# Kernel tuning notes

Measured on AMD Instinct MI355X. Metric: run time of the kernel, lower is better.

The kernel has to match this reference:

```python
import jax, jax.numpy as jnp
import numpy as np

EPS = 0.001

def batchnorm(x, gamma, beta):
    # x: [N, C, H, W]; training-mode batch statistics over (N, H, W), biased variance (torch BN)
    mean = jnp.mean(x, axis=(0, 2, 3), keepdims=True)
    var = jnp.mean(jnp.square(x - mean), axis=(0, 2, 3), keepdims=True)
    xn = (x - mean) * jax.lax.rsqrt(var + EPS)
    return xn * gamma[None, :, None, None] + beta[None, :, None, None]

def setup_inputs() -> dict:
    key = jax.random.key(0)
    ks = jax.random.split(key, 6)
    N, C, C2, H, W = 8, 256, 256, 96, 96
    num_heads, key_dim, value_dim = 8, 32, 32
    q_input = jax.random.normal(ks[0], (N, C, H, W), dtype=jnp.float32)
    kv = jax.random.normal(ks[1], (N, C2, H, W), dtype=jnp.float32)
    # 1x1 conv weights as matrices [out, in], kaiming-normal-ish scale
    Wq = jax.random.normal(ks[2], (key_dim * num_heads, C), dtype=jnp.float32) * np.sqrt(2.0 / C)
    Wk = jax.random.normal(ks[3], (key_dim * num_heads, C2), dtype=jnp.float32) * np.sqrt(2.0 / C2)
    Wv = jax.random.normal(ks[4], (value_dim * num_heads, C2), dtype=jnp.float32) * np.sqrt(2.0 / C2)
    Wp = jax.random.normal(ks[5], (C, value_dim * num_heads), dtype=jnp.float32) * np.sqrt(2.0 / (value_dim * num_heads))
    return {
        "q_input": q_input, "kv": kv,
        "Wq": Wq, "Wk": Wk, "Wv": Wv, "Wp": Wp,
        "q_gamma": jnp.ones((C,), jnp.float32), "q_beta": jnp.zeros((C,), jnp.float32),
        "kv_gamma": jnp.ones((C2,), jnp.float32), "kv_beta": jnp.zeros((C2,), jnp.float32),
    }

def reference(q_input, kv, Wq, Wk, Wv, Wp, q_gamma, q_beta, kv_gamma, kv_beta):
    NUM_HEADS, KEY_DIM, VALUE_DIM = 8, 32, 32
    n, C, q_h, q_w = q_input.shape
    _, C2, kv_h, kv_w = kv.shape
    Lq, Lk = q_h * q_w, kv_h * kv_w
    qn = batchnorm(q_input, q_gamma, q_beta)
    kvn = batchnorm(kv, kv_gamma, kv_beta)
    # 1x1 convs == channel matmuls; reshape to [n, heads, dim, L]
    queries = jnp.einsum('oc,nchw->nohw', Wq, qn).reshape(n, NUM_HEADS, KEY_DIM, Lq)
    keys = jnp.einsum('oc,nchw->nohw', Wk, kvn).reshape(n, NUM_HEADS, KEY_DIM, Lk)
    values = jnp.einsum('oc,nchw->nohw', Wv, kvn).reshape(n, NUM_HEADS, VALUE_DIM, Lk)
    key_sm = jax.nn.softmax(keys, axis=-1)        # softmax over kv spatial positions
    query_sm = jax.nn.softmax(queries, axis=2)    # softmax over key_dim channels
    # context[k,v] = sum_l key[k,l] * value[v,l]
    context = jnp.einsum('nhkl,nhvl->nhkv', key_sm, values)
    # attended[v,q] = sum_k context[k,v] * query[k,q]
    attended = jnp.einsum('nhkv,nhkq->nhvq', context, query_sm)
    aggregated = attended.reshape(n, NUM_HEADS * VALUE_DIM, Lq)
    reproj = jnp.einsum('cv,nvq->ncq', Wp, aggregated).reshape(n, C, q_h, q_w)
    return reproj + q_input
```

## Files before the change

kernel.cpp:

```cpp
#include <hip/hip_runtime.h>

#define L 9216
#define CNTF 73728.0f

#define F_DENOM 1024
#define F_CTX 3072
#define F_STATS 68608
#define B_M2 274432u
#define B_QSM 38023168u

#define O_WF 0u
#define O_BIAS 393216u

typedef float floatx4 __attribute__((ext_vector_type(4)));
typedef __bf16 bf16x8 __attribute__((ext_vector_type(8)));

__device__ __forceinline__ unsigned short f2bf(float f){
  return __builtin_bit_cast(unsigned short, (__bf16)f);
}
__device__ __forceinline__ unsigned pack2(float lo, float hi){
  return (unsigned)f2bf(lo) | ((unsigned)f2bf(hi) << 16);
}
__device__ __forceinline__ int swz(int r){ return (r ^ (r >> 4)) & 7; }
__device__ __forceinline__ int sw4(int r){ return (r ^ (r >> 4)) & 15; }

__device__ __forceinline__ void gload16(const void* g, void* l){
  __builtin_amdgcn_global_load_lds(
      (const __attribute__((address_space(1))) unsigned*)g,
      (__attribute__((address_space(3))) unsigned*)l, 16, 0, 0);
}

__global__ __launch_bounds__(256, 4) void k_stats(const float* __restrict__ q,
                                                  const float* __restrict__ kv,
                                                  float* __restrict__ ws){
  int b = blockIdx.x, t = threadIdx.x;
  int ten = b >> 11;
  int row = b & 2047;
  const float4* p = (const float4*)((ten ? kv : q) + (size_t)row * L);
  float4 v0 = p[t        ], v1 = p[t +  256], v2 = p[t +  512];
  float4 v3 = p[t +  768 ], v4 = p[t + 1024], v5 = p[t + 1280];
  float4 v6 = p[t + 1536 ], v7 = p[t + 1792], v8 = p[t + 2048];
  float s0 = v0.x+v0.y+v0.z+v0.w, q0 = v0.x*v0.x+v0.y*v0.y+v0.z*v0.z+v0.w*v0.w;
  float s1 = v1.x+v1.y+v1.z+v1.w, q1 = v1.x*v1.x+v1.y*v1.y+v1.z*v1.z+v1.w*v1.w;
  float s2 = v2.x+v2.y+v2.z+v2.w, q2 = v2.x*v2.x+v2.y*v2.y+v2.z*v2.z+v2.w*v2.w;
  s0 += v3.x+v3.y+v3.z+v3.w; q0 += v3.x*v3.x+v3.y*v3.y+v3.z*v3.z+v3.w*v3.w;
  s1 += v4.x+v4.y+v4.z+v4.w; q1 += v4.x*v4.x+v4.y*v4.y+v4.z*v4.z+v4.w*v4.w;
  s2 += v5.x+v5.y+v5.z+v5.w; q2 += v5.x*v5.x+v5.y*v5.y+v5.z*v5.z+v5.w*v5.w;
  s0 += v6.x+v6.y+v6.z+v6.w; q0 += v6.x*v6.x+v6.y*v6.y+v6.z*v6.z+v6.w*v6.w;
  s1 += v7.x+v7.y+v7.z+v7.w; q1 += v7.x*v7.x+v7.y*v7.y+v7.z*v7.z+v7.w*v7.w;
  s2 += v8.x+v8.y+v8.z+v8.w; q2 += v8.x*v8.x+v8.y*v8.y+v8.z*v8.z+v8.w*v8.w;
  float s = s0 + s1 + s2, ss = q0 + q1 + q2;
  #pragma unroll
  for (int off = 1; off < 64; off <<= 1){
    s += __shfl_xor(s, off); ss += __shfl_xor(ss, off);
  }
  __shared__ float r4[2][4];
  int w = t >> 6;
  if ((t & 63) == 0){ r4[0][w] = s; r4[1][w] = ss; }
  __syncthreads();
  if (t == 0){
    s  = r4[0][0]+r4[0][1]+r4[0][2]+r4[0][3];
    ss = r4[1][0]+r4[1][1]+r4[1][2]+r4[1][3];
    ws[F_STATS + ten*4096 + row] = s;
    ws[F_STATS + ten*4096 + 2048 + row] = ss;
  }
}

__global__ __launch_bounds__(256) void k_wfold(const float* __restrict__ W0,
    const float* __restrict__ W1, const float* __restrict__ W2,
    float* __restrict__ ws,
    const float* __restrict__ qg, const float* __restrict__ qb,
    const float* __restrict__ kg, const float* __restrict__ kb,
    char* __restrict__ outa){
  __shared__ float sc[256], sh[256];
  int b = blockIdx.x, r = threadIdx.x;
  int tsel = (b < 2) ? 1 : 0;
  {
    float s = 0.f, ssum = 0.f;
    #pragma unroll
    for (int n = 0; n < 8; ++n){
      s    += ws[F_STATS + tsel*4096 + n*256 + r];
      ssum += ws[F_STATS + tsel*4096 + 2048 + n*256 + r];
    }
    float m = s * (1.0f/CNTF);
    float vv = ssum * (1.0f/CNTF) - m*m;
    float g  = tsel ? kg[r] : qg[r];
    float be = tsel ? kb[r] : qb[r];
    float scv = rsqrtf(vv + 1e-3f) * g;
    sc[r] = scv; sh[r] = be - m*scv;
  }
  for (int j = 0; j < 88; ++j){
    int i = j*768 + b*256 + r;
    if (i < 67584) ws[F_DENOM + i] = 0.0f;
  }
  __syncthreads();
  const float* W = (b == 0) ? W0 : ((b == 1) ? W1 : W2);
  const float* wrow = W + (size_t)r * 256;
  int imgrow, biasidx;
  char* chunk;
  if (b < 2){
    int h = r >> 5;
    imgrow = (h >> 1)*128 + (h & 1)*64 + b*32 + (r & 31);
    biasidx = imgrow;
    chunk = outa + O_WF;
  } else {
    imgrow = r;
    biasidx = 512 + r;
    chunk = outa + O_WF + 262144;
  }
  int opl = imgrow >> 7, rl = imgrow & 127;
  float bias = 0.f;
  for (int kc = 0; kc < 4; ++kc){
    unsigned pk[8][4];
    #pragma unroll
    for (int g = 0; g < 8; ++g){
      float v[8];
      #pragma unroll
      for (int m = 0; m < 8; ++m){
        int k = kc*64 + g*8 + m;
        float w = wrow[k];
        v[m] = w * sc[k];
        bias = fmaf(w, sh[k], bias);
      }
      pk[g][0] = pack2(v[0], v[1]); pk[g][1] = pack2(v[2], v[3]);
      pk[g][2] = pack2(v[4], v[5]); pk[g][3] = pack2(v[6], v[7]);
    }
    #pragma unroll
    for (int g = 0; g < 8; ++g){
      int idx = (opl*4 + kc)*1024 + rl*8 + (g ^ swz(rl));
      *(uint4*)(chunk + (size_t)idx*16) =
          make_uint4(pk[g][0], pk[g][1], pk[g][2], pk[g][3]);
    }
  }
  ((float*)(outa + O_BIAS))[biasidx] = bias;
}

__global__ __launch_bounds__(256, 2) void k_fkv(
    const char* __restrict__ Af, const float* __restrict__ kv,
    const float* __restrict__ bias, float* __restrict__ ws)
{
  __shared__ __align__(16) ushort SH[128*128];
  ushort* As = SH;
  ushort* Bs = SH + 128*64;
  char*   EV = (char*)SH;
  const int t = threadIdx.x;
  const int lane = t & 63, wid = t >> 6;
  const int wr = wid >> 1, wc = wid & 1;
  const int bid = blockIdx.x;
  const int xcd = bid & 7, seq = bid >> 3;
  const int op = seq & 3;
  const int lpi = (seq >> 2) & 3;
  const int gid = xcd * 18 + (seq >> 4);
  const int lpg = gid % 18, n = gid / 18;
  const int l0 = (lpg*4 + lpi) * 128;
  const char* Achunk = Af + (size_t)op * 65536;
  const int cpair = t >> 3, lg = t & 7;
  const int lcol = lane & 15, lhi = lane >> 4;
  const int lrow4 = lhi * 4;

  float bv[4];
  #pragma unroll
  for (int of = 0; of < 4; ++of)
    bv[of] = bias[op*128 + wr*64 + of*16 + lcol];

  floatx4 c16[2] = {};
  floatx4 acc[4][4] = {};
  for (int kc = 0; kc < 4; ++kc){
    {
      const char* src = Achunk + kc*16384 + ((size_t)(wid*4*64 + lane))*16;
      ushort* dst = As + wid*4*512;
      gload16(src,        dst);
      gload16(src + 1024, dst + 512);
      gload16(src + 2048, dst + 1024);
      gload16(src + 3072, dst + 1536);
    }
    unsigned bu[16];
    {
      const float* Xa = kv + ((size_t)(n*256 + kc*64 + 2*cpair))*L + l0 + lg*16;
      const float* Xb = Xa + L;
      #pragma unroll
      for (int q = 0; q < 4; ++q){
        float4 a = ((const float4*)Xa)[q];
        float4 b = ((const float4*)Xb)[q];
        bu[4*q+0] = pack2(a.x, b.x);
        bu[4*q+1] = pack2(a.y, b.y);
        bu[4*q+2] = pack2(a.z, b.z);
        bu[4*q+3] = pack2(a.w, b.w);
      }
    }
    {
      int g = cpair >> 2, d = cpair & 3;
      #pragma unroll
      for (int j = 0; j < 16; ++j){
        int ll = lg*16 + j;
        *(unsigned*)((char*)Bs + ll*128 + ((g ^ swz(ll))*16) + d*4) = bu[j];
      }
    }
    __syncthreads();
    #pragma unroll
    for (int ks = 0; ks < 2; ++ks){
      bf16x8 af[4], bfr[4];
      #pragma unroll
      for (int mf = 0; mf < 4; ++mf){
        int row = wr*64 + mf*16 + lcol;
        int gq = (ks*4 + lhi) ^ swz(row);
        af[mf] = *(const bf16x8*)(As + row*64 + gq*8);
      }
      #pragma unroll
      for (int nf = 0; nf < 4; ++nf){
        int ll = wc*64 + nf*16 + lcol;
        int gq = (ks*4 + lhi) ^ swz(ll);
        bfr[nf] = *(const bf16x8*)(Bs + ll*64 + gq*8);
      }
      #pragma unroll
      for (int lf = 0; lf < 4; ++lf)
        #pragma unroll
        for (int of = 0; of < 4; ++of)
          acc[lf][of] = __builtin_amdgcn_mfma_f32_16x16x32_bf16(bfr[lf], af[of], acc[lf][of], 0, 0, 0);
    }
    __syncthreads();
  }

  #pragma unroll
  for (int lf = 0; lf < 4; ++lf)
    #pragma unroll
    for (int of = 0; of < 4; ++of)
      #pragma unroll
      for (int r = 0; r < 4; ++r){
        if (of < 2) acc[lf][of][r] = __expf(acc[lf][of][r] + bv[of]);
        else        acc[lf][of][r] += bv[of];
      }
  #pragma unroll
  for (int of = 0; of < 2; ++of){
    float s = 0.f;
    #pragma unroll
    for (int lf = 0; lf < 4; ++lf)
      #pragma unroll
      for (int r = 0; r < 4; ++r)
        s += acc[lf][of][r];
    s += __shfl_xor(s, 16);
    s += __shfl_xor(s, 32);
    if (lhi == 0)
      atomicAdd(ws + F_DENOM + (size_t)((n*8) + op*2 + wr)*32 + of*16 + lcol, s);
  }
  #pragma unroll
  for (int of = 0; of < 4; ++of){
    int row = wr*64 + of*16 + lcol;
    #pragma unroll
    for (int lf = 0; lf < 4; ++lf){
      int col = wc*64 + lf*16 + lrow4;
      int g = (col >> 3) ^ sw4(row);
      char* p = EV + row*256 + g*16 + (col & 7)*2;
      *(unsigned*)p       = pack2(acc[lf][of][0], acc[lf][of][1]);
      *(unsigned*)(p + 4) = pack2(acc[lf][of][2], acc[lf][of][3]);
    }
  }
  __syncthreads();
  #pragma unroll
  for (int kk = 0; kk < 4; ++kk){
    int gk = (kk*32 + lhi*8) >> 3;
    bf16x8 aE0, aE1, bV;
    {
      int row = wr*64 + lcol;
      aE0 = *(const bf16x8*)(EV + row*256 + ((gk ^ sw4(row))*16));
    }
    {
      int row = wr*64 + 16 + lcol;
      aE1 = *(const bf16x8*)(EV + row*256 + ((gk ^ sw4(row))*16));
    }
    {
      int row = wr*64 + 32 + wc*16 + lcol;
      bV = *(const bf16x8*)(EV + row*256 + ((gk ^ sw4(row))*16));
    }
    c16[0] = __builtin_amdgcn_mfma_f32_16x16x32_bf16(aE0, bV, c16[0], 0, 0, 0);
    c16[1] = __builtin_amdgcn_mfma_f32_16x16x32_bf16(aE1, bV, c16[1], 0, 0, 0);
  }

  float* ctxp = ws + F_CTX + (size_t)((n*8) + op*2 + wr)*1024;
  #pragma unroll
  for (int i0 = 0; i0 < 2; ++i0)
    #pragma unroll
    for (int r = 0; r < 4; ++r)
      atomicAdd(ctxp + (i0*16 + lrow4 + r)*32 + wc*16 + lcol, c16[i0][r]);
}

template<int MODE>
__global__ __launch_bounds__(256, 3) void k_gemm(
    const char* __restrict__ Af, size_t a_nstride,
    const void* __restrict__ Bsrc,
    const float* __restrict__ bias,
    void* __restrict__ outp, const float* __restrict__ xres,
    const float* __restrict__ Wp, float* __restrict__ wsf)
{
  __shared__ __align__(16) ushort SH[128*128];
  ushort* As = SH;
  ushort* Bs = SH + 128*64;
  const int t = threadIdx.x;
  const int bid = blockIdx.x;

  if (MODE == 1 && bid >= 1152){
    float (*cn)[33] = (float(*)[33])SH;
    int nh = bid - 1152;
    int n = nh >> 3, h = nh & 7;
    #pragma unroll
    for (int jj = 0; jj < 4; ++jj){
      int i = jj*256 + t;
      int k = i >> 5, v = i & 31;
      cn[k][v] = wsf[F_CTX + (size_t)nh*1024 + i] / wsf[F_DENOM + nh*32 + k];
    }
    __syncthreads();
    int c = t;
    const float* wrow = Wp + (size_t)c*256 + h*32;
    float w[32];
    #pragma unroll
    for (int v = 0; v < 32; ++v) w[v] = wrow[v];
    float s[32];
    #pragma unroll
    for (int k = 0; k < 32; ++k){
      float a = 0.f;
      #pragma unroll
      for (int v = 0; v < 32; ++v) a = fmaf(w[v], cn[k][v], a);
      s[k] = a;
    }
    char* base = (char*)wsf + B_M2 + (size_t)n*131072;
    int opl = c >> 7, rl = c & 127, kc = h >> 1;
    #pragma unroll
    for (int gg = 0; gg < 4; ++gg){
      int g = (h & 1)*4 + gg;
      uint4 u = make_uint4(pack2(s[gg*8+0], s[gg*8+1]), pack2(s[gg*8+2], s[gg*8+3]),
                           pack2(s[gg*8+4], s[gg*8+5]), pack2(s[gg*8+6], s[gg*8+7]));
      *(uint4*)(base + (size_t)((opl*4 + kc)*1024 + rl*8 + (g ^ swz(rl)))*16) = u;
    }
    return;
  }

  const int lane = t & 63, wid = t >> 6;
  const int wr = wid >> 1, wc = wid & 1;
  const int xcd = bid & 7, seq = bid >> 3;
  const int op = seq & 1;
  const int gid = xcd * 72 + (seq >> 1);
  const int lp = gid % 72, n = gid / 72;
  const int l0 = lp * 128, o0 = op * 128;
  const char* Achunk = Af + (size_t)n * a_nstride + (size_t)op * 65536;
  const char* Bn = (const char*)Bsrc + (size_t)n * 4718592;
  const int cpair = t >> 3, lg = t & 7;
  const int lcol = lane & 15, lhi = lane >> 4;
  const int r8 = lane >> 3, s8 = lane & 7;

  floatx4 acc[4][4] = {};

  for (int kc = 0; kc < 4; ++kc) {
    {
      const char* src = Achunk + kc*16384 + ((size_t)(wid*4*64 + lane))*16;
      ushort* dst = As + wid*4*512;
      gload16(src,        dst);
      gload16(src + 1024, dst + 512);
      gload16(src + 2048, dst + 1024);
      gload16(src + 3072, dst + 1536);
    }
    if (MODE == 2) {
      #pragma unroll
      for (int i = 0; i < 4; ++i){
        int rw = wid*32 + i*8 + r8;
        const char* src = Bn + (size_t)(l0 + rw)*512 + kc*128 + ((s8 ^ swz(rw))*16);
        gload16(src, Bs + (wid*32 + i*8)*64);
      }
    } else {
      unsigned bu[16];
      const float* Xa = (const float*)Bsrc + ((size_t)(n*256 + kc*64 + 2*cpair))*L + l0 + lg*16;
      const float* Xb = Xa + L;
      #pragma unroll
      for (int q = 0; q < 4; ++q) {
        float4 a = ((const float4*)Xa)[q];
        float4 b = ((const float4*)Xb)[q];
        bu[4*q+0] = pack2(a.x, b.x);
        bu[4*q+1] = pack2(a.y, b.y);
        bu[4*q+2] = pack2(a.z, b.z);
        bu[4*q+3] = pack2(a.w, b.w);
      }
      int g = cpair >> 2, d = cpair & 3;
      #pragma unroll
      for (int j = 0; j < 16; ++j){
        int ll = lg*16 + j;
        *(unsigned*)((char*)Bs + ll*128 + ((g ^ swz(ll))*16) + d*4) = bu[j];
      }
    }
    __syncthreads();
    #pragma unroll
    for (int ks = 0; ks < 2; ++ks) {
      bf16x8 af[4], bfr[4];
      #pragma unroll
      for (int mf = 0; mf < 4; ++mf) {
        int row = wr*64 + mf*16 + lcol;
        int gq = (ks*4 + lhi) ^ swz(row);
        af[mf] = *(const bf16x8*)(As + row*64 + gq*8);
      }
      #pragma unroll
      for (int nf = 0; nf < 4; ++nf) {
        int ll = wc*64 + nf*16 + lcol;
        int gq = (ks*4 + lhi) ^ swz(ll);
        bfr[nf] = *(const bf16x8*)(Bs + ll*64 + gq*8);
      }
      #pragma unroll
      for (int mf = 0; mf < 4; ++mf)
        #pragma unroll
        for (int nf = 0; nf < 4; ++nf)
          acc[mf][nf] = __builtin_amdgcn_mfma_f32_16x16x32_bf16(af[mf], bfr[nf], acc[mf][nf], 0, 0, 0);
    }
    __syncthreads();
  }

  const int lrow4 = lhi * 4;

  if (MODE == 1) {
    #pragma unroll
    for (int mf = 0; mf < 4; ++mf)
      #pragma unroll
      for (int r = 0; r < 4; ++r) {
        float bv = bias[o0 + wr*64 + mf*16 + lrow4 + r];
        #pragma unroll
        for (int nf = 0; nf < 4; ++nf)
          acc[mf][nf][r] = __expf(acc[mf][nf][r] + bv);
      }
    #pragma unroll
    for (int hg = 0; hg < 2; ++hg) {
      #pragma unroll
      for (int nf = 0; nf < 4; ++nf) {
        float s = 0.f;
        #pragma unroll
        for (int mh = 0; mh < 2; ++mh)
          #pragma unroll
          for (int r = 0; r < 4; ++r)
            s += acc[hg*2+mh][nf][r];
        s += __shfl_xor(s, 16);
        s += __shfl_xor(s, 32);
        float inv = 1.0f / s;
        #pragma unroll
        for (int mh = 0; mh < 2; ++mh)
          #pragma unroll
          for (int r = 0; r < 4; ++r)
            acc[hg*2+mh][nf][r] *= inv;
      }
    }
    ushort* Lst = SH;
    #pragma unroll
    for (int mf = 0; mf < 4; ++mf){
      int ol = wr*64 + mf*16 + lrow4;
      int och = ol >> 3;
      #pragma unroll
      for (int nf = 0; nf < 4; ++nf){
        int ll = wc*64 + nf*16 + lcol;
        unsigned w0 = pack2(acc[mf][nf][0], acc[mf][nf][1]);
        unsigned w1 = pack2(acc[mf][nf][2], acc[mf][nf][3]);
        char* p = (char*)Lst + ll*256 + ((och ^ sw4(ll))*16) + (ol & 7)*2;
        *(unsigned*)p = w0;
        *(unsigned*)(p + 4) = w1;
      }
    }
    __syncthreads();
    char* ob = (char*)outp + (size_t)(n*9216 + l0)*512 + o0*2;
    #pragma unroll
    for (int j = 0; j < 8; ++j){
      int flat = j*256 + t;
      int l = flat >> 4, seg = flat & 15;
      uint4 v = *(const uint4*)((const char*)Lst + l*256 + ((seg ^ sw4(l))*16));
      *(uint4*)(ob + (size_t)l*512 + seg*16) = v;
    }
  }

  if (MODE == 2) {
    float* outf = (float*)outp;
    #pragma unroll
    for (int mf = 0; mf < 4; ++mf)
      #pragma unroll
      for (int r = 0; r < 4; ++r) {
        int orow = o0 + wr*64 + mf*16 + lrow4 + r;
        size_t base = ((size_t)n*256 + orow)*L + l0 + wc*64 + lcol;
        #pragma unroll
        for (int nf = 0; nf < 4; ++nf) {
          size_t gi = base + (size_t)nf*16;
          outf[gi] = acc[mf][nf][r] + xres[gi];
        }
      }
  }
}

extern "C" void kernel_launch(void* const* d_in, const int* in_sizes, int n_in,
                              void* d_out, int out_size, void* d_ws, size_t ws_size,
                              hipStream_t stream)
{
  const float* q_in = (const float*)d_in[0];
  const float* kv   = (const float*)d_in[1];
  const float* Wq   = (const float*)d_in[2];
  const float* Wk   = (const float*)d_in[3];
  const float* Wv   = (const float*)d_in[4];
  const float* Wp   = (const float*)d_in[5];
  const float* qg   = (const float*)d_in[6];
  const float* qb   = (const float*)d_in[7];
  const float* kg   = (const float*)d_in[8];
  const float* kb   = (const float*)d_in[9];
  float* out = (float*)d_out;
  float* wsf = (float*)d_ws;
  char*  outa = (char*)d_out;
  const float* biasf = (const float*)(outa + O_BIAS);

  k_stats<<<dim3(4096), dim3(256), 0, stream>>>(q_in, kv, wsf);
  k_wfold<<<dim3(3),    dim3(256), 0, stream>>>(Wk, Wv, Wq, wsf, qg, qb, kg, kb, outa);
  k_fkv  <<<dim3(2304), dim3(256), 0, stream>>>(outa + O_WF, kv, biasf, wsf);
  k_gemm<1><<<dim3(1216), dim3(256), 0, stream>>>(outa + O_WF + 262144, 0, q_in,
      biasf + 512, (char*)d_ws + B_QSM, nullptr, Wp, wsf);
  k_gemm<2><<<dim3(1152), dim3(256), 0, stream>>>((char*)d_ws + B_M2, 131072,
      (char*)d_ws + B_QSM, nullptr, out, q_in, nullptr, wsf);
}
```

Baseline: 151.2 us.

## Move q batch statistics into the kv-GEMM launch and split weight folding

The q-input batchnorm statistics are no longer computed ahead of the kv path. They now run as extra blocks appended to the k_fkv launch, and the kv statistics keep their own kernel. The weight folding is split into a kv-only kernel before k_fkv and a q-only kernel after it, so the q stats pass can overlap with the kv projection GEMM instead of sitting on the critical path. The cost is one extra small launch, plus stats blocks that compete with GEMM blocks for bandwidth and occupancy.

```diff
diff --git a/kernel.cpp b/kernel.cpp
--- a/kernel.cpp
+++ b/kernel.cpp
@@ -30,84 +30,70 @@
       (__attribute__((address_space(3))) unsigned*)l, 16, 0, 0);
 }
 
-__global__ __launch_bounds__(256, 4) void k_stats(const float* __restrict__ q,
-                                                  const float* __restrict__ kv,
-                                                  float* __restrict__ ws){
-  int b = blockIdx.x, t = threadIdx.x;
-  int ten = b >> 11;
-  int row = b & 2047;
-  const float4* p = (const float4*)((ten ? kv : q) + (size_t)row * L);
-  float4 v0 = p[t        ], v1 = p[t +  256], v2 = p[t +  512];
-  float4 v3 = p[t +  768 ], v4 = p[t + 1024], v5 = p[t + 1280];
-  float4 v6 = p[t + 1536 ], v7 = p[t + 1792], v8 = p[t + 2048];
-  float s0 = v0.x+v0.y+v0.z+v0.w, q0 = v0.x*v0.x+v0.y*v0.y+v0.z*v0.z+v0.w*v0.w;
-  float s1 = v1.x+v1.y+v1.z+v1.w, q1 = v1.x*v1.x+v1.y*v1.y+v1.z*v1.z+v1.w*v1.w;
-  float s2 = v2.x+v2.y+v2.z+v2.w, q2 = v2.x*v2.x+v2.y*v2.y+v2.z*v2.z+v2.w*v2.w;
-  s0 += v3.x+v3.y+v3.z+v3.w; q0 += v3.x*v3.x+v3.y*v3.y+v3.z*v3.z+v3.w*v3.w;
-  s1 += v4.x+v4.y+v4.z+v4.w; q1 += v4.x*v4.x+v4.y*v4.y+v4.z*v4.z+v4.w*v4.w;
-  s2 += v5.x+v5.y+v5.z+v5.w; q2 += v5.x*v5.x+v5.y*v5.y+v5.z*v5.z+v5.w*v5.w;
-  s0 += v6.x+v6.y+v6.z+v6.w; q0 += v6.x*v6.x+v6.y*v6.y+v6.z*v6.z+v6.w*v6.w;
-  s1 += v7.x+v7.y+v7.z+v7.w; q1 += v7.x*v7.x+v7.y*v7.y+v7.z*v7.z+v7.w*v7.w;
-  s2 += v8.x+v8.y+v8.z+v8.w; q2 += v8.x*v8.x+v8.y*v8.y+v8.z*v8.z+v8.w*v8.w;
-  float s = s0 + s1 + s2, ss = q0 + q1 + q2;
+__device__ __forceinline__ void stats_row(const float* __restrict__ rowp,
+                                          float* __restrict__ outs,
+                                          float* __restrict__ outq,
+                                          float* __restrict__ red, int t){
+  const float4* p = (const float4*)rowp;
+  float4 v[9];
+  #pragma unroll
+  for (int j = 0; j < 9; ++j) v[j] = p[t + 256*j];
+  __builtin_amdgcn_sched_barrier(0);
+  float s = 0.f, ss = 0.f;
+  #pragma unroll
+  for (int j = 0; j < 9; ++j){
+    s  += v[j].x + v[j].y + v[j].z + v[j].w;
+    ss += v[j].x*v[j].x + v[j].y*v[j].y + v[j].z*v[j].z + v[j].w*v[j].w;
+  }
   #pragma unroll
   for (int off = 1; off < 64; off <<= 1){
     s += __shfl_xor(s, off); ss += __shfl_xor(ss, off);
   }
-  __shared__ float r4[2][4];
   int w = t >> 6;
-  if ((t & 63) == 0){ r4[0][w] = s; r4[1][w] = ss; }
+  if ((t & 63) == 0){ red[w] = s; red[4 + w] = ss; }
   __syncthreads();
   if (t == 0){
-    s  = r4[0][0]+r4[0][1]+r4[0][2]+r4[0][3];
-    ss = r4[1][0]+r4[1][1]+r4[1][2]+r4[1][3];
-    ws[F_STATS + ten*4096 + row] = s;
-    ws[F_STATS + ten*4096 + 2048 + row] = ss;
-  }
-}
-
-__global__ __launch_bounds__(256) void k_wfold(const float* __restrict__ W0,
-    const float* __restrict__ W1, const float* __restrict__ W2,
-    float* __restrict__ ws,
-    const float* __restrict__ qg, const float* __restrict__ qb,
+    *outs = red[0]+red[1]+red[2]+red[3];
+    *outq = red[4]+red[5]+red[6]+red[7];
+  }
+}
+
+__global__ __launch_bounds__(256) void k_statskv(const float* __restrict__ kv,
+                                                 float* __restrict__ ws){
+  __shared__ float red[8];
+  int b = blockIdx.x, t = threadIdx.x;
+  stats_row(kv + (size_t)b*L, &ws[F_STATS + 4096 + b],
+            &ws[F_STATS + 4096 + 2048 + b], red, t);
+}
+
+__global__ __launch_bounds__(256) void k_wfoldkv(const float* __restrict__ W0,
+    const float* __restrict__ W1, float* __restrict__ ws,
     const float* __restrict__ kg, const float* __restrict__ kb,
     char* __restrict__ outa){
   __shared__ float sc[256], sh[256];
   int b = blockIdx.x, r = threadIdx.x;
-  int tsel = (b < 2) ? 1 : 0;
   {
     float s = 0.f, ssum = 0.f;
     #pragma unroll
     for (int n = 0; n < 8; ++n){
-      s    += ws[F_STATS + tsel*4096 + n*256 + r];
-      ssum += ws[F_STATS + tsel*4096 + 2048 + n*256 + r];
+      s    += ws[F_STATS + 4096 + n*256 + r];
+      ssum += ws[F_STATS + 4096 + 2048 + n*256 + r];
     }
     float m = s * (1.0f/CNTF);
     float vv = ssum * (1.0f/CNTF) - m*m;
-    float g  = tsel ? kg[r] : qg[r];
-    float be = tsel ? kb[r] : qb[r];
-    float scv = rsqrtf(vv + 1e-3f) * g;
-    sc[r] = scv; sh[r] = be - m*scv;
-  }
-  for (int j = 0; j < 88; ++j){
-    int i = j*768 + b*256 + r;
+    float scv = rsqrtf(vv + 1e-3f) * kg[r];
+    sc[r] = scv; sh[r] = kb[r] - m*scv;
+  }
+  for (int j = 0; j < 132; ++j){
+    int i = j*512 + b*256 + r;
     if (i < 67584) ws[F_DENOM + i] = 0.0f;
   }
   __syncthreads();
-  const float* W = (b == 0) ? W0 : ((b == 1) ? W1 : W2);
+  const float* W = (b == 0) ? W0 : W1;
   const float* wrow = W + (size_t)r * 256;
-  int imgrow, biasidx;
-  char* chunk;
-  if (b < 2){
-    int h = r >> 5;
-    imgrow = (h >> 1)*128 + (h & 1)*64 + b*32 + (r & 31);
-    biasidx = imgrow;
-    chunk = outa + O_WF;
-  } else {
-    imgrow = r;
-    biasidx = 512 + r;
-    chunk = outa + O_WF + 262144;
-  }
+  int h = r >> 5;
+  int imgrow = (h >> 1)*128 + (h & 1)*64 + b*32 + (r & 31);
+  char* chunk = outa + O_WF;
   int opl = imgrow >> 7, rl = imgrow & 127;
   float bias = 0.f;
   for (int kc = 0; kc < 4; ++kc){
@@ -132,21 +118,78 @@
           make_uint4(pk[g][0], pk[g][1], pk[g][2], pk[g][3]);
     }
   }
-  ((float*)(outa + O_BIAS))[biasidx] = bias;
+  ((float*)(outa + O_BIAS))[imgrow] = bias;
+}
+
+__global__ __launch_bounds__(256) void k_wfoldq(const float* __restrict__ W2,
+    float* __restrict__ ws,
+    const float* __restrict__ qg, const float* __restrict__ qb,
+    char* __restrict__ outa){
+  __shared__ float sc[256], sh[256];
+  int r = threadIdx.x;
+  {
+    float s = 0.f, ssum = 0.f;
+    #pragma unroll
+    for (int n = 0; n < 8; ++n){
+      s    += ws[F_STATS + n*256 + r];
+      ssum += ws[F_STATS + 2048 + n*256 + r];
+    }
+    float m = s * (1.0f/CNTF);
+    float vv = ssum * (1.0f/CNTF) - m*m;
+    float scv = rsqrtf(vv + 1e-3f) * qg[r];
+    sc[r] = scv; sh[r] = qb[r] - m*scv;
+  }
+  __syncthreads();
+  const float* wrow = W2 + (size_t)r * 256;
+  char* chunk = outa + O_WF + 262144;
+  int opl = r >> 7, rl = r & 127;
+  float bias = 0.f;
+  for (int kc = 0; kc < 4; ++kc){
+    unsigned pk[8][4];
+    #pragma unroll
+    for (int g = 0; g < 8; ++g){
+      float v[8];
+      #pragma unroll
+      for (int m = 0; m < 8; ++m){
+        int k = kc*64 + g*8 + m;
+        float w = wrow[k];
+        v[m] = w * sc[k];
+        bias = fmaf(w, sh[k], bias);
+      }
+      pk[g][0] = pack2(v[0], v[1]); pk[g][1] = pack2(v[2], v[3]);
+      pk[g][2] = pack2(v[4], v[5]); pk[g][3] = pack2(v[6], v[7]);
+    }
+    #pragma unroll
+    for (int g = 0; g < 8; ++g){
+      int idx = (opl*4 + kc)*1024 + rl*8 + (g ^ swz(rl));
+      *(uint4*)(chunk + (size_t)idx*16) =
+          make_uint4(pk[g][0], pk[g][1], pk[g][2], pk[g][3]);
+    }
+  }
+  ((float*)(outa + O_BIAS))[512 + r] = bias;
 }
 
 __global__ __launch_bounds__(256, 2) void k_fkv(
     const char* __restrict__ Af, const float* __restrict__ kv,
+    const float* __restrict__ q_in,
     const float* __restrict__ bias, float* __restrict__ ws)
 {
   __shared__ __align__(16) ushort SH[128*128];
+  const int t = threadIdx.x;
+  const int bid = blockIdx.x;
+
+  if (bid >= 2304){
+    int sb = bid - 2304;
+    stats_row(q_in + (size_t)sb*L, &ws[F_STATS + sb],
+              &ws[F_STATS + 2048 + sb], (float*)SH, t);
+    return;
+  }
+
   ushort* As = SH;
   ushort* Bs = SH + 128*64;
   char*   EV = (char*)SH;
-  const int t = threadIdx.x;
   const int lane = t & 63, wid = t >> 6;
   const int wr = wid >> 1, wc = wid & 1;
-  const int bid = blockIdx.x;
   const int xcd = bid & 7, seq = bid >> 3;
   const int op = seq & 3;
   const int lpi = (seq >> 2) & 3;
@@ -504,9 +547,10 @@
   char*  outa = (char*)d_out;
   const float* biasf = (const float*)(outa + O_BIAS);
 
-  k_stats<<<dim3(4096), dim3(256), 0, stream>>>(q_in, kv, wsf);
-  k_wfold<<<dim3(3),    dim3(256), 0, stream>>>(Wk, Wv, Wq, wsf, qg, qb, kg, kb, outa);
-  k_fkv  <<<dim3(2304), dim3(256), 0, stream>>>(outa + O_WF, kv, biasf, wsf);
+  k_statskv<<<dim3(2048), dim3(256), 0, stream>>>(kv, wsf);
+  k_wfoldkv<<<dim3(2),   dim3(256), 0, stream>>>(Wk, Wv, wsf, kg, kb, outa);
+  k_fkv    <<<dim3(4352), dim3(256), 0, stream>>>(outa + O_WF, kv, q_in, biasf, wsf);
+  k_wfoldq <<<dim3(1),   dim3(256), 0, stream>>>(Wq, wsf, qg, qb, outa);
   k_gemm<1><<<dim3(1216), dim3(256), 0, stream>>>(outa + O_WF + 262144, 0, q_in,
       biasf + 512, (char*)d_ws + B_QSM, nullptr, Wp, wsf);
   k_gemm<2><<<dim3(1152), dim3(256), 0, stream>>>((char*)d_ws + B_M2, 131072,
```

Measured after the change: 167.2 us. +10.6%, slower.
